# Performance work log

Measured on AMD Instinct MI355X. Metric: run time of the kernel, lower is better.

The kernel has to match this reference:

```python
import jax, jax.numpy as jnp
import numpy as np

N_NODES = 20000
N_EDGES = 200000
D_IN, D_H1, D_H2, D_OUT = 1433, 1000, 500, 7


def setup_inputs() -> dict:
    key = jax.random.key(0)
    ks = jax.random.split(key, 8)
    features = jax.random.normal(ks[0], (N_NODES, D_IN), dtype=jnp.float32)
    src = jax.random.randint(ks[1], (N_EDGES,), 0, N_NODES)
    dst = jax.random.randint(ks[2], (N_EDGES,), 0, N_NODES)
    W1 = jax.random.normal(ks[3], (D_IN, D_H1), dtype=jnp.float32) * 0.02
    b1 = jnp.zeros((D_H1,), dtype=jnp.float32)
    W2 = jax.random.normal(ks[4], (D_H1, D_H2), dtype=jnp.float32) * 0.02
    b2 = jnp.zeros((D_H2,), dtype=jnp.float32)
    W3 = jax.random.normal(ks[5], (D_H2, D_OUT), dtype=jnp.float32) * 0.02
    b3 = jnp.zeros((D_OUT,), dtype=jnp.float32)
    return {"features": features, "src": src, "dst": dst,
            "W1": W1, "b1": b1, "W2": W2, "b2": b2, "W3": W3, "b3": b3}


def reference(features, src, dst, W1, b1, W2, b2, W3, b3):
    N = features.shape[0]

    def agg(x):  # sum_tensors over incoming neighbors: h_i = sum_{(j->i) in E} x_j
        return jax.ops.segment_sum(x[src], dst, num_segments=N)

    # GCN layer 1: aggregate -> linear -> relu
    x = jax.nn.relu(agg(features) @ W1 + b1)       # [N, 1000]
    # GCN layer 2: aggregate -> linear -> relu (dropout = identity in eval)
    x = jax.nn.relu(agg(x) @ W2 + b2)              # [N, 500]
    # output linear -> relu (dropout = identity in eval)
    x = jax.nn.relu(x @ W3 + b3)                   # [N, 7]
    return x
```

## Files before the change

### kernel.cpp

```cpp
#include <hip/hip_runtime.h>
#include <hip/hip_bf16.h>
#include <hip/hip_cooperative_groups.h>

namespace cg = cooperative_groups;


#define N_NODES 20000
#define N_EDGES 200000
#define D_IN    1433
#define D_H1    1000
#define D_H2    500
#define D_OUT   7

#define MPAD    20096
#define K1PAD   1472
#define N1PAD   1024
#define K2PAD   1024
#define N2PAD   512
#define H1STR   1024
#define H2STR   512
#define MBLK    157
#define SCAN_N  (N_NODES + 1)
#define CSR_NB  20
#define CSR_T   (CSR_NB * 1024)
#define TB1     ((N1PAD / 32) * (K1PAD / 32))
#define TB2     ((N2PAD / 32) * (K2PAD / 32))

typedef __attribute__((ext_vector_type(8))) short short8;
typedef __attribute__((ext_vector_type(8))) unsigned short ushort8_t;
typedef __attribute__((ext_vector_type(4))) float f32x4;

__device__ __forceinline__ unsigned short bf16_rne(float x) {
    unsigned int u = __float_as_uint(x);
    u = (u + 0x7FFFu + ((u >> 16) & 1u)) >> 16;
    return (unsigned short)u;
}
__device__ __forceinline__ float bf16_up(unsigned short h) {
    return __uint_as_float((unsigned int)h << 16);
}

__device__ __forceinline__ void gl_lds16(const unsigned short* g, unsigned short* lds) {
    __builtin_amdgcn_global_load_lds(
        (const __attribute__((address_space(1))) unsigned int*)g,
        (__attribute__((address_space(3))) unsigned int*)lds, 16, 0, 0);
}

__global__ __launch_bounds__(256) void prep(const float* __restrict__ F,
                                            unsigned int* __restrict__ Fout,
                                            const float* __restrict__ W1,
                                            unsigned short* __restrict__ W1T,
                                            const float* __restrict__ W2,
                                            unsigned short* __restrict__ W2T) {
    __shared__ float tile[32][33];
    const int bid = blockIdx.x, t = threadIdx.x;
    if (bid < MPAD) {
        const float* fr = F + (size_t)bid * D_IN;
        bool live = bid < N_NODES;
        for (int kk = t; kk < K1PAD / 2; kk += 256) {
            int k0 = kk * 2;
            float a = (live && k0     < D_IN) ? fr[k0]     : 0.f;
            float b = (live && k0 + 1 < D_IN) ? fr[k0 + 1] : 0.f;
            Fout[(size_t)bid * (K1PAD / 2) + kk] =
                (unsigned int)bf16_rne(a) | ((unsigned int)bf16_rne(b) << 16);
        }
        return;
    }
    const float* src; unsigned short* dst;
    int SR, SC, DR, DC, bx, by;
    if (bid < MPAD + TB1) {
        int l = bid - MPAD;
        bx = l % (N1PAD / 32); by = l / (N1PAD / 32);
        src = W1; dst = W1T; SR = D_IN; SC = D_H1; DR = N1PAD; DC = K1PAD;
    } else {
        int l = bid - MPAD - TB1;
        bx = l % (N2PAD / 32); by = l / (N2PAD / 32);
        src = W2; dst = W2T; SR = D_H1; SC = D_H2; DR = N2PAD; DC = K2PAD;
    }
    const int c0 = bx * 32, r0 = by * 32;
    const int tx = t & 31, ty = t >> 5;
    #pragma unroll
    for (int p = 0; p < 4; ++p) {
        int r = r0 + ty + p * 8, c = c0 + tx;
        tile[ty + p * 8][tx] = (r < SR && c < SC) ? src[(size_t)r * SC + c] : 0.f;
    }
    __syncthreads();
    #pragma unroll
    for (int p = 0; p < 4; ++p) {
        int dr = c0 + ty + p * 8;
        int dc = r0 + tx;
        if (dr < DR && dc < DC) dst[(size_t)dr * DC + dc] = bf16_rne(tile[tx][ty + p * 8]);
    }
}

__global__ __launch_bounds__(1024) void csr_build(const int* __restrict__ src,
                                                  const int* __restrict__ dst,
                                                  int* __restrict__ offs,
                                                  int* __restrict__ cursor,
                                                  int* __restrict__ srcs,
                                                  int* __restrict__ bsum) {
    cg::grid_group grid = cg::this_grid();
    __shared__ int wsum[16];
    const int t = threadIdx.x, bid = blockIdx.x;
    const int tid = bid * 1024 + t;

    if (tid < SCAN_N) offs[tid] = 0;
    grid.sync();

    const int4* dst4 = (const int4*)dst;
    const int4* src4 = (const int4*)src;
    for (int q = tid; q * 4 < N_EDGES; q += CSR_T) {
        int4 d = dst4[q];
        atomicAdd(&offs[d.x + 1], 1);
        atomicAdd(&offs[d.y + 1], 1);
        atomicAdd(&offs[d.z + 1], 1);
        atomicAdd(&offs[d.w + 1], 1);
    }
    grid.sync();

    const int lane = t & 63, wv = t >> 6;
    int v = (tid < SCAN_N) ? offs[tid] : 0;
    #pragma unroll
    for (int s = 1; s < 64; s <<= 1) {
        int u = __shfl_up(v, s, 64);
        if (lane >= s) v += u;
    }
    if (lane == 63) wsum[wv] = v;
    __syncthreads();
    int prefix = 0;
    for (int k = 0; k < wv; ++k) prefix += wsum[k];
    v += prefix;
    if (t == 1023) bsum[bid] = v;
    grid.sync();

    int add = 0;
    for (int k = 0; k < bid; ++k) add += bsum[k];
    v += add;
    if (tid < SCAN_N) offs[tid] = v;
    if (tid < N_NODES) cursor[tid] = v;
    grid.sync();

    for (int q = tid; q * 4 < N_EDGES; q += CSR_T) {
        int4 d = dst4[q];
        int4 s = src4[q];
        int p0 = atomicAdd(&cursor[d.x], 1);
        int p1 = atomicAdd(&cursor[d.y], 1);
        int p2 = atomicAdd(&cursor[d.z], 1);
        int p3 = atomicAdd(&cursor[d.w], 1);
        srcs[p0] = s.x; srcs[p1] = s.y; srcs[p2] = s.z; srcs[p3] = s.w;
    }
}

template <int KPAD, int NB>
__global__ __launch_bounds__(256) void gemm_mfma(const unsigned short* __restrict__ A,
                                                 const unsigned short* __restrict__ B,
                                                 unsigned short* __restrict__ C,
                                                 int M, int OSTR) {
    __shared__ __align__(16) unsigned short sA[128 * 64];
    __shared__ __align__(16) unsigned short sB[128 * 64];
    const int bid = blockIdx.x;
    const int xcd = bid & 7;
    const int tt  = bid >> 3;
    const int nb  = tt % NB;
    const int mb  = (tt / NB) * 8 + xcd;
    if (mb >= MBLK) return;

    const int t = threadIdx.x;
    const int w = t >> 6, lane = t & 63;
    const int m0 = mb * 128, n0 = nb * 128;
    const int wm = (w >> 1) * 64, wn = (w & 1) * 64;

    const int srowo = lane >> 3;
    const int skc   = ((lane & 7) ^ srowo) * 8;
    const int mrow = lane & 15, quad = lane >> 4;

    const unsigned short* Aptr = A + (size_t)(m0 + srowo) * KPAD + skc;
    const unsigned short* Bptr = B + (size_t)(n0 + srowo) * KPAD + skc;

    f32x4 acc[4][4] = {};

    for (int k0 = 0; k0 < KPAD; k0 += 64) {
        #pragma unroll
        for (int c = 0; c < 4; ++c) {
            const int rbase = c * 32 + w * 8;
            gl_lds16(Aptr + (size_t)rbase * KPAD, &sA[rbase * 64]);
            gl_lds16(Bptr + (size_t)rbase * KPAD, &sB[rbase * 64]);
        }
        Aptr += 64; Bptr += 64;
        __syncthreads();

        #pragma unroll
        for (int s = 0; s < 2; ++s) {
            short8 af[4], bf[4];
            #pragma unroll
            for (int mt = 0; mt < 4; ++mt) {
                int r = wm + mt * 16 + mrow;
                af[mt] = *(const short8*)&sA[r * 64 + (((s * 4 + quad) ^ (mrow & 7)) * 8)];
            }
            #pragma unroll
            for (int nt = 0; nt < 4; ++nt) {
                int r = wn + nt * 16 + mrow;
                bf[nt] = *(const short8*)&sB[r * 64 + (((s * 4 + quad) ^ (mrow & 7)) * 8)];
            }
            #pragma unroll
            for (int mt = 0; mt < 4; ++mt)
                #pragma unroll
                for (int nt = 0; nt < 4; ++nt)
                    acc[mt][nt] = __builtin_amdgcn_mfma_f32_16x16x32_bf16(
                        af[mt], bf[nt], acc[mt][nt], 0, 0, 0);
        }
        __syncthreads();
    }

    #pragma unroll
    for (int mt = 0; mt < 4; ++mt) {
        int m = m0 + wm + mt * 16 + quad * 4;
        #pragma unroll
        for (int nt = 0; nt < 4; ++nt) {
            int n = n0 + wn + nt * 16 + mrow;
            #pragma unroll
            for (int r = 0; r < 4; ++r)
                if (m + r < M) C[(size_t)(m + r) * OSTR + n] = bf16_rne(acc[mt][nt][r]);
        }
    }
}

__global__ __launch_bounds__(128) void agg1_bf16(const unsigned short* __restrict__ H,
                                                 const int* __restrict__ offs,
                                                 const int* __restrict__ srcs,
                                                 const float* __restrict__ bias,
                                                 unsigned short* __restrict__ X) {
    const int i = blockIdx.x, t = threadIdx.x;
    const bool active = t < 125;
    const int tc = active ? t : 124;
    ushort8_t o = (ushort8_t)0;
    if (i < N_NODES) {
        const int beg = offs[i], end = offs[i + 1];
        const unsigned short* Hc = H + tc * 8;
        float s[8] = {};
        int e = beg;
        for (; e + 8 <= end; e += 8) {
            int j0 = srcs[e],     j1 = srcs[e + 1], j2 = srcs[e + 2], j3 = srcs[e + 3];
            int j4 = srcs[e + 4], j5 = srcs[e + 5], j6 = srcs[e + 6], j7 = srcs[e + 7];
            ushort8_t v0 = *(const ushort8_t*)(Hc + (size_t)j0 * H1STR);
            ushort8_t v1 = *(const ushort8_t*)(Hc + (size_t)j1 * H1STR);
            ushort8_t v2 = *(const ushort8_t*)(Hc + (size_t)j2 * H1STR);
            ushort8_t v3 = *(const ushort8_t*)(Hc + (size_t)j3 * H1STR);
            ushort8_t v4 = *(const ushort8_t*)(Hc + (size_t)j4 * H1STR);
            ushort8_t v5 = *(const ushort8_t*)(Hc + (size_t)j5 * H1STR);
            ushort8_t v6 = *(const ushort8_t*)(Hc + (size_t)j6 * H1STR);
            ushort8_t v7 = *(const ushort8_t*)(Hc + (size_t)j7 * H1STR);
            #pragma unroll
            for (int u = 0; u < 8; ++u) {
                float t0 = (bf16_up(v0[u]) + bf16_up(v1[u])) +
                           (bf16_up(v2[u]) + bf16_up(v3[u]));
                float t1 = (bf16_up(v4[u]) + bf16_up(v5[u])) +
                           (bf16_up(v6[u]) + bf16_up(v7[u]));
                s[u] += t0 + t1;
            }
        }
        for (; e + 4 <= end; e += 4) {
            int j0 = srcs[e], j1 = srcs[e + 1], j2 = srcs[e + 2], j3 = srcs[e + 3];
            ushort8_t v0 = *(const ushort8_t*)(Hc + (size_t)j0 * H1STR);
            ushort8_t v1 = *(const ushort8_t*)(Hc + (size_t)j1 * H1STR);
            ushort8_t v2 = *(const ushort8_t*)(Hc + (size_t)j2 * H1STR);
            ushort8_t v3 = *(const ushort8_t*)(Hc + (size_t)j3 * H1STR);
            #pragma unroll
            for (int u = 0; u < 8; ++u)
                s[u] += (bf16_up(v0[u]) + bf16_up(v1[u])) +
                        (bf16_up(v2[u]) + bf16_up(v3[u]));
        }
        for (; e < end; ++e) {
            ushort8_t v = *(const ushort8_t*)(Hc + (size_t)srcs[e] * H1STR);
            #pragma unroll
            for (int u = 0; u < 8; ++u) s[u] += bf16_up(v[u]);
        }
        if (active) {
            #pragma unroll
            for (int u = 0; u < 8; ++u)
                o[u] = bf16_rne(fmaxf(s[u] + bias[t * 8 + u], 0.f));
        }
    }
    *(ushort8_t*)(X + (size_t)i * K2PAD + t * 8) = o;
}

__global__ __launch_bounds__(64) void agg2_out(const unsigned short* __restrict__ H,
                                               const int* __restrict__ offs,
                                               const int* __restrict__ srcs,
                                               const float* __restrict__ b2,
                                               const float* __restrict__ W3,
                                               const float* __restrict__ b3,
                                               float* __restrict__ out) {
    const int i = blockIdx.x, t = threadIdx.x;
    const int tc = t < 63 ? t : 62;
    const int beg = offs[i], end = offs[i + 1];
    const unsigned short* Hc = H + tc * 8;
    float s[8] = {};
    int e = beg;
    for (; e + 8 <= end; e += 8) {
        int j0 = srcs[e],     j1 = srcs[e + 1], j2 = srcs[e + 2], j3 = srcs[e + 3];
        int j4 = srcs[e + 4], j5 = srcs[e + 5], j6 = srcs[e + 6], j7 = srcs[e + 7];
        ushort8_t v0 = *(const ushort8_t*)(Hc + (size_t)j0 * H2STR);
        ushort8_t v1 = *(const ushort8_t*)(Hc + (size_t)j1 * H2STR);
        ushort8_t v2 = *(const ushort8_t*)(Hc + (size_t)j2 * H2STR);
        ushort8_t v3 = *(const ushort8_t*)(Hc + (size_t)j3 * H2STR);
        ushort8_t v4 = *(const ushort8_t*)(Hc + (size_t)j4 * H2STR);
        ushort8_t v5 = *(const ushort8_t*)(Hc + (size_t)j5 * H2STR);
        ushort8_t v6 = *(const ushort8_t*)(Hc + (size_t)j6 * H2STR);
        ushort8_t v7 = *(const ushort8_t*)(Hc + (size_t)j7 * H2STR);
        #pragma unroll
        for (int u = 0; u < 8; ++u) {
            float t0 = (bf16_up(v0[u]) + bf16_up(v1[u])) +
                       (bf16_up(v2[u]) + bf16_up(v3[u]));
            float t1 = (bf16_up(v4[u]) + bf16_up(v5[u])) +
                       (bf16_up(v6[u]) + bf16_up(v7[u]));
            s[u] += t0 + t1;
        }
    }
    for (; e + 4 <= end; e += 4) {
        int j0 = srcs[e], j1 = srcs[e + 1], j2 = srcs[e + 2], j3 = srcs[e + 3];
        ushort8_t v0 = *(const ushort8_t*)(Hc + (size_t)j0 * H2STR);
        ushort8_t v1 = *(const ushort8_t*)(Hc + (size_t)j1 * H2STR);
        ushort8_t v2 = *(const ushort8_t*)(Hc + (size_t)j2 * H2STR);
        ushort8_t v3 = *(const ushort8_t*)(Hc + (size_t)j3 * H2STR);
        #pragma unroll
        for (int u = 0; u < 8; ++u)
            s[u] += (bf16_up(v0[u]) + bf16_up(v1[u])) +
                    (bf16_up(v2[u]) + bf16_up(v3[u]));
    }
    for (; e < end; ++e) {
        ushort8_t v = *(const ushort8_t*)(Hc + (size_t)srcs[e] * H2STR);
        #pragma unroll
        for (int u = 0; u < 8; ++u) s[u] += bf16_up(v[u]);
    }

    float acc[D_OUT] = {};
    if (t < 63) {
        #pragma unroll
        for (int u = 0; u < 8; ++u) {
            int col = t * 8 + u;
            if (col < D_H2) {
                float x = fmaxf(s[u] + b2[col], 0.f);
                const float* wr = W3 + (size_t)col * D_OUT;
                #pragma unroll
                for (int j = 0; j < D_OUT; ++j) acc[j] += x * wr[j];
            }
        }
    }
    #pragma unroll
    for (int j = 0; j < D_OUT; ++j)
        #pragma unroll
        for (int off = 32; off; off >>= 1) acc[j] += __shfl_down(acc[j], off);
    if (t == 0) {
        #pragma unroll
        for (int j = 0; j < D_OUT; ++j)
            out[(size_t)i * D_OUT + j] = fmaxf(acc[j] + b3[j], 0.f);
    }
}

extern "C" void kernel_launch(void* const* d_in, const int* in_sizes, int n_in,
                              void* d_out, int out_size, void* d_ws, size_t ws_size,
                              hipStream_t stream) {
    const float* features = (const float*)d_in[0];
    const int*   src      = (const int*)d_in[1];
    const int*   dst      = (const int*)d_in[2];
    const float* W1       = (const float*)d_in[3];
    const float* b1       = (const float*)d_in[4];
    const float* W2       = (const float*)d_in[5];
    const float* b2       = (const float*)d_in[6];
    const float* W3       = (const float*)d_in[7];
    const float* b3       = (const float*)d_in[8];
    float* out = (float*)d_out;

    char* ws = (char*)d_ws;
    unsigned short* Fbf  = (unsigned short*)(ws + 0);
    unsigned short* X1bf = (unsigned short*)(ws + 0);
    unsigned short* H1   = (unsigned short*)(ws + 59162624);
    unsigned short* H2   = (unsigned short*)(ws + 59162624);
    unsigned short* W1T  = (unsigned short*)(ws + 100122624);
    unsigned short* W2T  = (unsigned short*)(ws + 103137280);
    int* offs   = (int*)(ws + 100122624);
    int* cursor = (int*)(ws + 100202752);
    int* bsum   = (int*)(ws + 100282752);
    int* srcs   = (int*)(ws + 100282880);

    prep<<<MPAD + TB1 + TB2, 256, 0, stream>>>(
        features, (unsigned int*)Fbf, W1, W1T, W2, W2T);

    gemm_mfma<K1PAD, N1PAD / 128><<<8 * (N1PAD / 128) * 20, 256, 0, stream>>>(
        Fbf, W1T, H1, N_NODES, N1PAD);

    void* cargs[] = {(void*)&src, (void*)&dst, (void*)&offs,
                     (void*)&cursor, (void*)&srcs, (void*)&bsum};
    hipLaunchCooperativeKernel((void*)csr_build, dim3(CSR_NB), dim3(1024),
                               cargs, 0, stream);

    agg1_bf16<<<MPAD, 128, 0, stream>>>(H1, offs, srcs, b1, X1bf);

    gemm_mfma<K2PAD, N2PAD / 128><<<8 * (N2PAD / 128) * 20, 256, 0, stream>>>(
        X1bf, W2T, H2, N_NODES, N2PAD);

    agg2_out<<<N_NODES, 64, 0, stream>>>(H2, offs, srcs, b2, W3, b3, out);
}
```

Baseline: 488.4 us.

## Replace cooperative CSR build with fused counting, single-block scan and fill kernel

Removes the 20-block cooperative csr_build kernel and its four grid-wide syncs. Edge-degree counting now rides in the existing prep kernel, a single 1024-thread block does the prefix scan, and a separate one-thread-per-edge kernel scatters source indices. The scan's offsets array doubles as the fill cursor, so aggregation kernels now read segment bounds as offs[i-1]..offs[i]. This drops the cursor and block-sum buffers, and the srcs buffer reuses the W1T workspace once the first GEMM has finished with it. The cost is extra atomics inside prep, a serial single-block scan and one more launch.

```diff
diff --git a/kernel.cpp b/kernel.cpp
--- a/kernel.cpp
+++ b/kernel.cpp
@@ -1,8 +1,5 @@
 #include <hip/hip_runtime.h>
 #include <hip/hip_bf16.h>
-#include <hip/hip_cooperative_groups.h>
-
-namespace cg = cooperative_groups;
 
 
 #define N_NODES 20000
@@ -21,10 +18,9 @@
 #define H2STR   512
 #define MBLK    157
 #define SCAN_N  (N_NODES + 1)
-#define CSR_NB  20
-#define CSR_T   (CSR_NB * 1024)
 #define TB1     ((N1PAD / 32) * (K1PAD / 32))
 #define TB2     ((N2PAD / 32) * (K2PAD / 32))
+#define CNTB    ((N_EDGES + 255) / 256)
 
 typedef __attribute__((ext_vector_type(8))) short short8;
 typedef __attribute__((ext_vector_type(8))) unsigned short ushort8_t;
@@ -50,10 +46,14 @@
                                             const float* __restrict__ W1,
                                             unsigned short* __restrict__ W1T,
                                             const float* __restrict__ W2,
-                                            unsigned short* __restrict__ W2T) {
+                                            unsigned short* __restrict__ W2T,
+                                            const int* __restrict__ dst,
+                                            int* __restrict__ offs) {
     __shared__ float tile[32][33];
     const int bid = blockIdx.x, t = threadIdx.x;
     if (bid < MPAD) {
+        int e = bid * 256 + t;
+        if (e < N_EDGES) atomicAdd(&offs[dst[e] + 1], 1);
         const float* fr = F + (size_t)bid * D_IN;
         bool live = bid < N_NODES;
         for (int kk = t; kk < K1PAD / 2; kk += 256) {
@@ -65,16 +65,16 @@
         }
         return;
     }
-    const float* src; unsigned short* dst;
+    const float* src; unsigned short* dstp;
     int SR, SC, DR, DC, bx, by;
     if (bid < MPAD + TB1) {
         int l = bid - MPAD;
         bx = l % (N1PAD / 32); by = l / (N1PAD / 32);
-        src = W1; dst = W1T; SR = D_IN; SC = D_H1; DR = N1PAD; DC = K1PAD;
+        src = W1; dstp = W1T; SR = D_IN; SC = D_H1; DR = N1PAD; DC = K1PAD;
     } else {
         int l = bid - MPAD - TB1;
         bx = l % (N2PAD / 32); by = l / (N2PAD / 32);
-        src = W2; dst = W2T; SR = D_H1; SC = D_H2; DR = N2PAD; DC = K2PAD;
+        src = W2; dstp = W2T; SR = D_H1; SC = D_H2; DR = N2PAD; DC = K2PAD;
     }
     const int c0 = bx * 32, r0 = by * 32;
     const int tx = t & 31, ty = t >> 5;
@@ -88,65 +88,49 @@
     for (int p = 0; p < 4; ++p) {
         int dr = c0 + ty + p * 8;
         int dc = r0 + tx;
-        if (dr < DR && dc < DC) dst[(size_t)dr * DC + dc] = bf16_rne(tile[tx][ty + p * 8]);
-    }
-}
-
-__global__ __launch_bounds__(1024) void csr_build(const int* __restrict__ src,
-                                                  const int* __restrict__ dst,
-                                                  int* __restrict__ offs,
-                                                  int* __restrict__ cursor,
-                                                  int* __restrict__ srcs,
-                                                  int* __restrict__ bsum) {
-    cg::grid_group grid = cg::this_grid();
+        if (dr < DR && dc < DC) dstp[(size_t)dr * DC + dc] = bf16_rne(tile[tx][ty + p * 8]);
+    }
+}
+
+__global__ __launch_bounds__(1024) void scan_csr(int* __restrict__ offs) {
     __shared__ int wsum[16];
-    const int t = threadIdx.x, bid = blockIdx.x;
-    const int tid = bid * 1024 + t;
-
-    if (tid < SCAN_N) offs[tid] = 0;
-    grid.sync();
-
-    const int4* dst4 = (const int4*)dst;
-    const int4* src4 = (const int4*)src;
-    for (int q = tid; q * 4 < N_EDGES; q += CSR_T) {
-        int4 d = dst4[q];
-        atomicAdd(&offs[d.x + 1], 1);
-        atomicAdd(&offs[d.y + 1], 1);
-        atomicAdd(&offs[d.z + 1], 1);
-        atomicAdd(&offs[d.w + 1], 1);
-    }
-    grid.sync();
-
-    const int lane = t & 63, wv = t >> 6;
-    int v = (tid < SCAN_N) ? offs[tid] : 0;
+    const int t = threadIdx.x, lane = t & 63, wv = t >> 6;
+    const int base = t * 20;
+    int v[20];
+    int run = 0;
+    #pragma unroll
+    for (int k = 0; k < 20; ++k) {
+        int i = base + k;
+        int x = (i < SCAN_N) ? offs[i] : 0;
+        run += x;
+        v[k] = run;
+    }
+    const int tot = run;
+    int w = tot;
     #pragma unroll
     for (int s = 1; s < 64; s <<= 1) {
-        int u = __shfl_up(v, s, 64);
-        if (lane >= s) v += u;
-    }
-    if (lane == 63) wsum[wv] = v;
+        int u = __shfl_up(w, s, 64);
+        if (lane >= s) w += u;
+    }
+    if (lane == 63) wsum[wv] = w;
     __syncthreads();
-    int prefix = 0;
+    int prefix = w - tot;
     for (int k = 0; k < wv; ++k) prefix += wsum[k];
-    v += prefix;
-    if (t == 1023) bsum[bid] = v;
-    grid.sync();
-
-    int add = 0;
-    for (int k = 0; k < bid; ++k) add += bsum[k];
-    v += add;
-    if (tid < SCAN_N) offs[tid] = v;
-    if (tid < N_NODES) cursor[tid] = v;
-    grid.sync();
-
-    for (int q = tid; q * 4 < N_EDGES; q += CSR_T) {
-        int4 d = dst4[q];
-        int4 s = src4[q];
-        int p0 = atomicAdd(&cursor[d.x], 1);
-        int p1 = atomicAdd(&cursor[d.y], 1);
-        int p2 = atomicAdd(&cursor[d.z], 1);
-        int p3 = atomicAdd(&cursor[d.w], 1);
-        srcs[p0] = s.x; srcs[p1] = s.y; srcs[p2] = s.z; srcs[p3] = s.w;
+    #pragma unroll
+    for (int k = 0; k < 20; ++k) {
+        int i = base + k;
+        if (i < SCAN_N) offs[i] = prefix + v[k];
+    }
+}
+
+__global__ __launch_bounds__(256) void fill_csr(const int* __restrict__ src,
+                                                const int* __restrict__ dst,
+                                                int* __restrict__ offs,
+                                                int* __restrict__ srcs) {
+    int e = blockIdx.x * 256 + threadIdx.x;
+    if (e < N_EDGES) {
+        int pos = atomicAdd(&offs[dst[e]], 1);
+        srcs[pos] = src[e];
     }
 }
 
@@ -234,7 +218,8 @@
     const int tc = active ? t : 124;
     ushort8_t o = (ushort8_t)0;
     if (i < N_NODES) {
-        const int beg = offs[i], end = offs[i + 1];
+        const int end = offs[i];
+        const int beg = i ? offs[i - 1] : 0;
         const unsigned short* Hc = H + tc * 8;
         float s[8] = {};
         int e = beg;
@@ -292,7 +277,8 @@
                                                float* __restrict__ out) {
     const int i = blockIdx.x, t = threadIdx.x;
     const int tc = t < 63 ? t : 62;
-    const int beg = offs[i], end = offs[i + 1];
+    const int end = offs[i];
+    const int beg = i ? offs[i - 1] : 0;
     const unsigned short* Hc = H + tc * 8;
     float s[8] = {};
     int e = beg;
@@ -378,21 +364,20 @@
     unsigned short* H2   = (unsigned short*)(ws + 59162624);
     unsigned short* W1T  = (unsigned short*)(ws + 100122624);
     unsigned short* W2T  = (unsigned short*)(ws + 103137280);
-    int* offs   = (int*)(ws + 100122624);
-    int* cursor = (int*)(ws + 100202752);
-    int* bsum   = (int*)(ws + 100282752);
-    int* srcs   = (int*)(ws + 100282880);
+    int* srcs   = (int*)(ws + 100122624);
+    int* offs   = (int*)(ws + 104185856);
+
+    hipMemsetAsync(offs, 0, SCAN_N * sizeof(int), stream);
 
     prep<<<MPAD + TB1 + TB2, 256, 0, stream>>>(
-        features, (unsigned int*)Fbf, W1, W1T, W2, W2T);
+        features, (unsigned int*)Fbf, W1, W1T, W2, W2T, dst, offs);
+
+    scan_csr<<<1, 1024, 0, stream>>>(offs);
 
     gemm_mfma<K1PAD, N1PAD / 128><<<8 * (N1PAD / 128) * 20, 256, 0, stream>>>(
         Fbf, W1T, H1, N_NODES, N1PAD);
 
-    void* cargs[] = {(void*)&src, (void*)&dst, (void*)&offs,
-                     (void*)&cursor, (void*)&srcs, (void*)&bsum};
-    hipLaunchCooperativeKernel((void*)csr_build, dim3(CSR_NB), dim3(1024),
-                               cargs, 0, stream);
+    fill_csr<<<CNTB, 256, 0, stream>>>(src, dst, offs, srcs);
 
     agg1_bf16<<<MPAD, 128, 0, stream>>>(H1, offs, srcs, b1, X1bf);
 
```

Result: faster. 419.3 us (-14.1%).
